# Kernel tuning notes

Hardware: AMD Instinct MI355X
Metric: run time of the kernel (lower is better)

The kernel has to match this reference:

```python
import jax, jax.numpy as jnp
import numpy as np

N, L, C, H, W, HEAD = 16, 256, 512, 32, 32, 16

def setup_inputs() -> dict:
    key = jax.random.key(0)
    ks = jax.random.split(key, 8)
    s = 0.02  # weight init scale
    return {
        "feature": jax.random.normal(ks[0], (N, C, H, W), jnp.float32),
        "token": jax.random.normal(ks[1], (N, L, C), jnp.float32),
        "wq": jax.random.normal(ks[2], (C, C), jnp.float32) * s,
        "bq": jax.random.normal(ks[3], (C,), jnp.float32) * s,
        "wk": jax.random.normal(ks[4], (C, C), jnp.float32) * s,
        "bk": jax.random.normal(ks[5], (C,), jnp.float32) * s,
        "wv": jax.random.normal(ks[6], (C, C), jnp.float32) * s,
        "bv": jax.random.normal(ks[7], (C,), jnp.float32) * s,
    }

def reference(feature, token, wq, bq, wk, bk, wv, bv):
    n, c, hgt, wid = feature.shape
    h = HEAD
    d = c // h
    l = token.shape[1]
    scale = jnp.asarray(np.sqrt(c / h), feature.dtype)
    tok = token.transpose(0, 2, 1)  # (N, C, L)
    # 1x1 conv projections == per-position GEMMs
    v = (jnp.einsum('ncl,dc->ndl', tok, wv) + bv[None, :, None]).reshape(n, h, d, l)
    k = (jnp.einsum('ncl,dc->ndl', tok, wk) + bk[None, :, None]).reshape(n, h, d, l)
    q = (jnp.einsum('nchw,dc->ndhw', feature, wq) + bq[None, :, None, None])
    q = q.reshape(n, h, d, hgt * wid).transpose(0, 1, 3, 2)  # (N, h, HW, d)
    scores = jnp.einsum('nhqd,nhdl->nhql', q, k) / scale  # (N, h, HW, L)
    coef = jax.nn.softmax(scores, axis=-1)
    proj = jnp.einsum('nhdl,nhql->nhdq', v, coef)  # (N, h, d, HW)
    return feature + proj.reshape(n, c, hgt, wid)
```

## Files before the change

### kernel.cpp

```cpp
#include <hip/hip_runtime.h>
#include <hip/hip_bf16.h>

#define N_ 16
#define L_ 256
#define C_ 512
#define HW_ 1024
#define HEADS_ 16
#define DH_ 32

typedef unsigned short u16;
typedef unsigned int u32;
typedef __attribute__((ext_vector_type(8))) short short8_t;
typedef __attribute__((ext_vector_type(4))) float f32x4;

__device__ __forceinline__ u16 f2bs(float f) {
    union { float f; u32 i; } x; x.f = f;
    u32 r = x.i + 0x7fffu + ((x.i >> 16) & 1u);
    return (u16)(r >> 16);
}
__device__ __forceinline__ u32 cvt_pk_bf16(float lo, float hi) {
    u32 r;
    asm("v_cvt_pk_bf16_f32 %0, %1, %2" : "=v"(r) : "v"(lo), "v"(hi));
    return r;
}
#define AS1(p) (const __attribute__((address_space(1))) void*)(p)
#define AS3(p) (__attribute__((address_space(3))) void*)(p)

__global__ __launch_bounds__(256) void prep_kernel(
    const float* __restrict__ token, const float* __restrict__ wq,
    const float* __restrict__ wk, const float* __restrict__ wv,
    const float* __restrict__ feature,
    u16* __restrict__ tokb, u16* __restrict__ wqb,
    u16* __restrict__ wkb, u16* __restrict__ wvb,
    u16* __restrict__ Ftb)
{
    __shared__ float LT[64][67];
    const int t = threadIdx.x;

    if (blockIdx.x < 2816) {
        const int idx = blockIdx.x * 256 + t;
        const float* s; u16* d; int off;
        if (idx < 524288)            { s = token; d = tokb; off = idx; }
        else if (idx < 524288+65536) { s = wq; d = wqb; off = idx - 524288; }
        else if (idx < 524288+131072){ s = wk; d = wkb; off = idx - 524288 - 65536; }
        else                         { s = wv; d = wvb; off = idx - 524288 - 131072; }
        float4 v = ((const float4*)s)[off];
        ushort4 w;
        w.x = f2bs(v.x); w.y = f2bs(v.y); w.z = f2bs(v.z); w.w = f2bs(v.w);
        ((ushort4*)d)[off] = w;
    } else {
        const int tidx = blockIdx.x - 2816;
        const int pb = tidx & 15, cb = (tidx >> 4) & 7, n = tidx >> 7;
        const int c0 = cb * 64, pos0 = pb * 64;

        #pragma unroll
        for (int r = 0; r < 4; ++r) {
            const int c = r * 16 + (t >> 4);
            const int p = (t & 15) * 4;
            float4 v = *(const float4*)&feature[
                ((size_t)n * C_ + c0 + c) * HW_ + pos0 + p];
            LT[c][p] = v.x; LT[c][p+1] = v.y; LT[c][p+2] = v.z; LT[c][p+3] = v.w;
        }
        __syncthreads();
        #pragma unroll
        for (int rep = 0; rep < 2; ++rep) {
            const int pos = (t >> 3) + rep * 32;
            const int c = (t & 7) * 8;
            u16 tmp[8];
            #pragma unroll
            for (int j = 0; j < 8; ++j) tmp[j] = f2bs(LT[c + j][pos]);
            *(short8_t*)&Ftb[(size_t)(n * HW_ + pos0 + pos) * C_ + c0 + c] =
                *(short8_t*)tmp;
        }
    }
}

__global__ __launch_bounds__(256) void gemm_kernel(
    const u16* __restrict__ Ftb, const u16* __restrict__ tokb,
    const u16* __restrict__ wqb, const u16* __restrict__ wkb,
    const u16* __restrict__ wvb,
    const float* __restrict__ bq, const float* __restrict__ bk,
    const float* __restrict__ bv,
    u16* __restrict__ Qout, u16* __restrict__ Kout, u16* __restrict__ Vt)
{
    __shared__ __align__(16) unsigned char smem[65536];

    const int t = threadIdx.x;
    const int lane = t & 63, wid = t >> 6;
    const int i16 = lane & 15, g = lane >> 4;
    const int r8 = t >> 3, gr = t & 7;

    if (blockIdx.x < 256) {
        const int xcd = blockIdx.x & 7, j = blockIdx.x >> 3;
        const int m0 = (xcd * 4 + (j & 3)) * 128;
        const int n0 = (j >> 2) * 64;
        const int wm = wid >> 1, wn = wid & 1;
        u16 (*LTo)[72] = (u16(*)[72])smem;

        f32x4 ak[4][2], av[4][2];
        #pragma unroll
        for (int mt = 0; mt < 4; ++mt)
            #pragma unroll
            for (int nt = 0; nt < 2; ++nt) {
                ak[mt][nt] = (f32x4){0.f, 0.f, 0.f, 0.f};
                av[mt][nt] = (f32x4){0.f, 0.f, 0.f, 0.f};
            }

        #define KV_STAGE(buf, c0) { \
            _Pragma("unroll") \
            for (int p = 0; p < 4; ++p) { \
                const int row = p * 32 + r8; \
                __builtin_amdgcn_global_load_lds( \
                    AS1(tokb + (size_t)(m0 + row) * C_ + (c0) + ((gr ^ (row & 7)) << 3)), \
                    AS3(smem + (buf) * 32768 + (p * 32 + wid * 8) * 128), 16, 0, 0); } \
            _Pragma("unroll") \
            for (int p = 0; p < 2; ++p) { \
                const int row = p * 32 + r8; \
                const int gs = (gr ^ (row & 7)) << 3; \
                __builtin_amdgcn_global_load_lds( \
                    AS1(wkb + (size_t)(n0 + row) * C_ + (c0) + gs), \
                    AS3(smem + (buf) * 32768 + 16384 + (p * 32 + wid * 8) * 128), 16, 0, 0); \
                __builtin_amdgcn_global_load_lds( \
                    AS1(wvb + (size_t)(n0 + row) * C_ + (c0) + gs), \
                    AS3(smem + (buf) * 32768 + 24576 + (p * 32 + wid * 8) * 128), 16, 0, 0); } }

        KV_STAGE(0, 0);
        __syncthreads();
        #pragma unroll
        for (int cs = 0; cs < 8; ++cs) {
            const int cur = cs & 1;
            if (cs < 7) KV_STAGE(cur ^ 1, (cs + 1) * 64);
            const u16* Tok = (const u16*)(smem + cur * 32768);
            const u16* Bk  = (const u16*)(smem + cur * 32768 + 16384);
            const u16* Bv  = (const u16*)(smem + cur * 32768 + 24576);
            #pragma unroll
            for (int ks = 0; ks < 2; ++ks) {
                short8_t a[4], bbk[2], bbv[2];
                #pragma unroll
                for (int mt = 0; mt < 4; ++mt) {
                    const int m = wm * 64 + mt * 16 + i16;
                    a[mt] = *(const short8_t*)&Tok[m * 64 + ((((ks << 2) | g) ^ (m & 7)) << 3)];
                }
                #pragma unroll
                for (int nt = 0; nt < 2; ++nt) {
                    const int d = wn * 32 + nt * 16 + i16;
                    const int sw = d * 64 + ((((ks << 2) | g) ^ (d & 7)) << 3);
                    bbk[nt] = *(const short8_t*)&Bk[sw];
                    bbv[nt] = *(const short8_t*)&Bv[sw];
                }
                #pragma unroll
                for (int mt = 0; mt < 4; ++mt)
                    #pragma unroll
                    for (int nt = 0; nt < 2; ++nt) {
                        ak[mt][nt] = __builtin_amdgcn_mfma_f32_16x16x32_bf16(
                            a[mt], bbk[nt], ak[mt][nt], 0, 0, 0);
                        av[mt][nt] = __builtin_amdgcn_mfma_f32_16x16x32_bf16(
                            a[mt], bbv[nt], av[mt][nt], 0, 0, 0);
                    }
            }
            __syncthreads();
        }
        const int nb = m0 >> 8, l0 = m0 & 255;
        const size_t vtbase = (size_t)nb * C_ * L_;
        #pragma unroll
        for (int nt = 0; nt < 2; ++nt) {
            const int d = n0 + wn * 32 + nt * 16 + i16;
            const float bb = bv[d];
            #pragma unroll
            for (int mt = 0; mt < 4; ++mt) {
                ushort4 w;
                w.x = f2bs(av[mt][nt][0] + bb);
                w.y = f2bs(av[mt][nt][1] + bb);
                w.z = f2bs(av[mt][nt][2] + bb);
                w.w = f2bs(av[mt][nt][3] + bb);
                const int l = l0 + wm * 64 + mt * 16 + g * 4;
                *(ushort4*)&Vt[vtbase + (size_t)d * L_ + l] = w;
            }
        }
        __syncthreads();
        #pragma unroll
        for (int nt = 0; nt < 2; ++nt) {
            const int col = wn * 32 + nt * 16 + i16;
            const float bb = bk[n0 + col];
            #pragma unroll
            for (int mt = 0; mt < 4; ++mt)
                #pragma unroll
                for (int r = 0; r < 4; ++r)
                    LTo[wm * 64 + mt * 16 + g * 4 + r][col] = f2bs(ak[mt][nt][r] + bb);
        }
        __syncthreads();
        #pragma unroll
        for (int rep = 0; rep < 4; ++rep) {
            const int m = (t >> 3) + rep * 32;
            const int cs2 = (t & 7) * 8;
            *(short8_t*)&Kout[(size_t)(m0 + m) * C_ + n0 + cs2] = *(short8_t*)&LTo[m][cs2];
        }
    } else {
        const int qid = blockIdx.x - 256;
        const int xcd = qid & 7, loc = qid >> 3;
        const int m0 = (xcd * 16 + (loc & 15)) * 128;
        const int n0 = (loc >> 4) * 128;
        const int wm = wid >> 1, wn = wid & 1;
        u16 (*LTo)[136] = (u16(*)[136])smem;

        f32x4 aq[4][4];
        #pragma unroll
        for (int mt = 0; mt < 4; ++mt)
            #pragma unroll
            for (int nt = 0; nt < 4; ++nt)
                aq[mt][nt] = (f32x4){0.f, 0.f, 0.f, 0.f};

        #define Q_STAGE(buf, c0) { \
            _Pragma("unroll") \
            for (int p = 0; p < 4; ++p) { \
                const int row = p * 32 + r8; \
                const int gs = (gr ^ (row & 7)) << 3; \
                __builtin_amdgcn_global_load_lds( \
                    AS1(Ftb + (size_t)(m0 + row) * C_ + (c0) + gs), \
                    AS3(smem + (buf) * 32768 + (p * 32 + wid * 8) * 128), 16, 0, 0); \
                __builtin_amdgcn_global_load_lds( \
                    AS1(wqb + (size_t)(n0 + row) * C_ + (c0) + gs), \
                    AS3(smem + (buf) * 32768 + 16384 + (p * 32 + wid * 8) * 128), 16, 0, 0); } }

        Q_STAGE(0, 0);
        __syncthreads();
        #pragma unroll
        for (int cs = 0; cs < 8; ++cs) {
            const int cur = cs & 1;
            if (cs < 7) Q_STAGE(cur ^ 1, (cs + 1) * 64);
            const u16* Ft = (const u16*)(smem + cur * 32768);
            const u16* Bq = (const u16*)(smem + cur * 32768 + 16384);
            #pragma unroll
            for (int ks = 0; ks < 2; ++ks) {
                short8_t a[4], b[4];
                #pragma unroll
                for (int mt = 0; mt < 4; ++mt) {
                    const int m = wm * 64 + mt * 16 + i16;
                    a[mt] = *(const short8_t*)&Ft[m * 64 + ((((ks << 2) | g) ^ (m & 7)) << 3)];
                }
                #pragma unroll
                for (int nt = 0; nt < 4; ++nt) {
                    const int d = wn * 64 + nt * 16 + i16;
                    b[nt] = *(const short8_t*)&Bq[d * 64 + ((((ks << 2) | g) ^ (d & 7)) << 3)];
                }
                #pragma unroll
                for (int mt = 0; mt < 4; ++mt)
                    #pragma unroll
                    for (int nt = 0; nt < 4; ++nt)
                        aq[mt][nt] = __builtin_amdgcn_mfma_f32_16x16x32_bf16(
                            a[mt], b[nt], aq[mt][nt], 0, 0, 0);
            }
            __syncthreads();
        }
        #pragma unroll
        for (int half = 0; half < 2; ++half) {
            __syncthreads();
            if (wm == half) {
                #pragma unroll
                for (int nt = 0; nt < 4; ++nt) {
                    const int col = wn * 64 + nt * 16 + i16;
                    const float bb = bq[n0 + col];
                    #pragma unroll
                    for (int mt = 0; mt < 4; ++mt)
                        #pragma unroll
                        for (int r = 0; r < 4; ++r)
                            LTo[mt * 16 + g * 4 + r][col] = f2bs(aq[mt][nt][r] + bb);
                }
            }
            __syncthreads();
            #pragma unroll
            for (int rep = 0; rep < 4; ++rep) {
                const int row = rep * 16 + (t >> 4);
                const int col = (t & 15) * 8;
                *(short8_t*)&Qout[(size_t)(m0 + half * 64 + row) * C_ + n0 + col] =
                    *(short8_t*)&LTo[row][col];
            }
        }
    }
}

__global__ __launch_bounds__(256) void attn_kernel(
    const u16* __restrict__ Qws, const u16* __restrict__ Kws,
    const u16* __restrict__ Vws, const float* __restrict__ feature,
    float* __restrict__ out)
{
    __shared__ __align__(16) unsigned char smem[32768];

    const int t = threadIdx.x;
    const int wid = t >> 6, lane = t & 63;
    const int i16 = lane & 15, g = lane >> 4;
    const int pt = blockIdx.x, h = blockIdx.y, n = blockIdx.z;
    const int pos0 = pt * 64;
    const size_t qbase = ((size_t)n * HW_ + pos0) * C_ + h * DH_;
    const size_t kbase = ((size_t)n * L_) * C_ + h * DH_;
    const size_t vbase = (size_t)n * C_ * L_ + (size_t)h * DH_ * L_;

    const int q = wid * 16 + i16;

    short8_t bq = *(const short8_t*)&Qws[qbase + (size_t)q * C_ + g * 8];

    #pragma unroll
    for (int p = 0; p < 4; ++p) {
        const int kg = (lane & 3) ^ ((lane >> 3) & 3);
        const int kr = wid * 64 + p * 16 + (lane >> 2);
        const u16* ksrc = Kws + kbase + (size_t)kr * C_ + kg * 8;
        __builtin_amdgcn_global_load_lds(AS1(ksrc),
            AS3(smem + wid * 4096 + p * 1024), 16, 0, 0);
        const int vd = wid * 8 + p * 2 + (lane >> 5);
        const u16* vsrc = Vws + vbase + (size_t)vd * L_ + ((lane & 31) ^ (vd & 7)) * 8;
        __builtin_amdgcn_global_load_lds(AS1(vsrc),
            AS3(smem + 16384 + wid * 4096 + p * 1024), 16, 0, 0);
    }
    __syncthreads();

    const int kgr = g ^ ((i16 >> 1) & 3);
    f32x4 s[16];
    #pragma unroll
    for (int nf = 0; nf < 16; ++nf) {
        short8_t a = *(const short8_t*)(smem + (nf * 16 + i16) * 64 + kgr * 16);
        f32x4 z = {0.f, 0.f, 0.f, 0.f};
        s[nf] = __builtin_amdgcn_mfma_f32_16x16x32_bf16(a, bq, z, 0, 0, 0);
    }

    float mm[16], sm[16];
    #pragma unroll
    for (int nf = 0; nf < 16; ++nf)
        mm[nf] = fmaxf(fmaxf(s[nf][0], s[nf][1]), fmaxf(s[nf][2], s[nf][3]));
    #pragma unroll
    for (int st = 8; st >= 1; st >>= 1)
        #pragma unroll
        for (int i = 0; i < 8; ++i)
            if (i < st) mm[i] = fmaxf(mm[i], mm[i + st]);
    float m = mm[0];
    m = fmaxf(m, __shfl_xor(m, 16));
    m = fmaxf(m, __shfl_xor(m, 32));

    const float K2 = 0.25506288f;
    #pragma unroll
    for (int nf = 0; nf < 16; ++nf) {
        #pragma unroll
        for (int r = 0; r < 4; ++r) s[nf][r] = exp2f((s[nf][r] - m) * K2);
        sm[nf] = (s[nf][0] + s[nf][1]) + (s[nf][2] + s[nf][3]);
    }
    #pragma unroll
    for (int st = 8; st >= 1; st >>= 1)
        #pragma unroll
        for (int i = 0; i < 8; ++i)
            if (i < st) sm[i] += sm[i + st];
    float ssum = sm[0];
    ssum += __shfl_xor(ssum, 16);
    ssum += __shfl_xor(ssum, 32);
    const float pinv = 1.0f / ssum;

    __syncthreads();

    f32x4 o0 = {0.f, 0.f, 0.f, 0.f}, o1 = {0.f, 0.f, 0.f, 0.f};
    const int e7 = i16 & 7;

    #pragma unroll
    for (int hb = 0; hb < 2; ++hb) {
        #pragma unroll
        for (int nfp = 0; nfp < 8; ++nfp) {
            const int nf = hb * 8 + nfp;
            #pragma unroll
            for (int w = 0; w < 2; ++w) {
                u32 pw = cvt_pk_bf16(s[nf][2 * w] * pinv, s[nf][2 * w + 1] * pinv);
                const int gran = (nfp * 2 + (g >> 1)) ^ e7;
                *(u32*)(smem + q * 256 + gran * 16 + ((g & 1) * 2 + w) * 4) = pw;
            }
        }
        __syncthreads();
        #pragma unroll
        for (int ks = 0; ks < 4; ++ks) {
            short8_t pb = *(const short8_t*)(smem + q * 256 + (((ks * 4 + g) ^ e7) * 16));
            const int vg = (((hb * 4 + ks) * 4 + g) ^ e7) * 16;
            short8_t va0 = *(const short8_t*)(smem + 16384 + i16 * 512 + vg);
            short8_t va1 = *(const short8_t*)(smem + 16384 + (16 + i16) * 512 + vg);
            o0 = __builtin_amdgcn_mfma_f32_16x16x32_bf16(va0, pb, o0, 0, 0, 0);
            o1 = __builtin_amdgcn_mfma_f32_16x16x32_bf16(va1, pb, o1, 0, 0, 0);
        }
        if (hb == 0) __syncthreads();
    }

    const size_t obase = ((size_t)n * C_ + h * DH_) * HW_ + pos0 + q;
    #pragma unroll
    for (int r = 0; r < 4; ++r) {
        const size_t oa = obase + (size_t)(g * 4 + r) * HW_;
        out[oa] = feature[oa] + o0[r];
        const size_t ob = obase + (size_t)(16 + g * 4 + r) * HW_;
        out[ob] = feature[ob] + o1[r];
    }
}

extern "C" void kernel_launch(void* const* d_in, const int* in_sizes, int n_in,
                              void* d_out, int out_size, void* d_ws, size_t ws_size,
                              hipStream_t stream)
{
    const float* feature = (const float*)d_in[0];
    const float* token   = (const float*)d_in[1];
    const float* wq      = (const float*)d_in[2];
    const float* bq      = (const float*)d_in[3];
    const float* wk      = (const float*)d_in[4];
    const float* bk      = (const float*)d_in[5];
    const float* wv      = (const float*)d_in[6];
    const float* bv      = (const float*)d_in[7];
    float* out = (float*)d_out;

    u16* Qws = (u16*)d_ws;
    u16* Kws = Qws + (size_t)N_ * HW_ * C_;
    u16* Vws = Kws + (size_t)N_ * L_ * C_;

    char* ob = (char*)d_out;
    u16* Ftb  = (u16*)ob;
    u16* tokb = (u16*)(ob + (16u << 20));
    u16* wkb  = (u16*)(ob + (20u << 20));
    u16* wvb  = (u16*)(ob + (20u << 20) + 524288);
    u16* wqb  = (u16*)(ob + (21u << 20));

    prep_kernel<<<dim3(4864), 256, 0, stream>>>(token, wq, wk, wv, feature,
                                                tokb, wqb, wkb, wvb, Ftb);
    gemm_kernel<<<dim3(768), 256, 0, stream>>>(Ftb, tokb, wqb, wkb, wvb,
                                               bq, bk, bv, Qws, Kws, Vws);
    attn_kernel<<<dim3(16, 16, 16), 256, 0, stream>>>(Qws, Kws, Vws, feature, out);
}
```

Before: 71.43 us.

## Fuse K/V projection with fp32-to-bf16 conversion into prep kernel

The K/V projection GEMM moves into the prep kernel and reads fp32 token and weights directly, converting to bf16 while staging into shared memory. This removes the separate bf16 copies of token, wk and wv and their global round trip. The Q GEMM becomes its own kernel. The fused K/V path drops the async global_load_lds double buffering in favour of synchronous register-staged loads, so it may overlap memory with compute less well. It also now runs concurrently with the feature transpose blocks.

Result: slower. 78.95 us (+10.5%).

```diff
diff --git a/kernel.cpp b/kernel.cpp
--- a/kernel.cpp
+++ b/kernel.cpp
@@ -23,33 +23,33 @@
     asm("v_cvt_pk_bf16_f32 %0, %1, %2" : "=v"(r) : "v"(lo), "v"(hi));
     return r;
 }
+__device__ __forceinline__ void cvt8(const float* __restrict__ src, void* dst) {
+    float4 lo = *(const float4*)src;
+    float4 hi = *(const float4*)(src + 4);
+    union { u32 w[4]; short8_t v; } pk;
+    pk.w[0] = cvt_pk_bf16(lo.x, lo.y);
+    pk.w[1] = cvt_pk_bf16(lo.z, lo.w);
+    pk.w[2] = cvt_pk_bf16(hi.x, hi.y);
+    pk.w[3] = cvt_pk_bf16(hi.z, hi.w);
+    *(short8_t*)dst = pk.v;
+}
 #define AS1(p) (const __attribute__((address_space(1))) void*)(p)
 #define AS3(p) (__attribute__((address_space(3))) void*)(p)
 
-__global__ __launch_bounds__(256) void prep_kernel(
-    const float* __restrict__ token, const float* __restrict__ wq,
-    const float* __restrict__ wk, const float* __restrict__ wv,
-    const float* __restrict__ feature,
-    u16* __restrict__ tokb, u16* __restrict__ wqb,
-    u16* __restrict__ wkb, u16* __restrict__ wvb,
-    u16* __restrict__ Ftb)
+__global__ __launch_bounds__(256) void prep_kv_kernel(
+    const float* __restrict__ feature, const float* __restrict__ token,
+    const float* __restrict__ wq, const float* __restrict__ wk,
+    const float* __restrict__ wv, const float* __restrict__ bk,
+    const float* __restrict__ bv,
+    u16* __restrict__ Ftb, u16* __restrict__ wqb,
+    u16* __restrict__ Kout, u16* __restrict__ Vt)
 {
-    __shared__ float LT[64][67];
+    __shared__ __align__(16) unsigned char smem[32768];
     const int t = threadIdx.x;
 
-    if (blockIdx.x < 2816) {
-        const int idx = blockIdx.x * 256 + t;
-        const float* s; u16* d; int off;
-        if (idx < 524288)            { s = token; d = tokb; off = idx; }
-        else if (idx < 524288+65536) { s = wq; d = wqb; off = idx - 524288; }
-        else if (idx < 524288+131072){ s = wk; d = wkb; off = idx - 524288 - 65536; }
-        else                         { s = wv; d = wvb; off = idx - 524288 - 131072; }
-        float4 v = ((const float4*)s)[off];
-        ushort4 w;
-        w.x = f2bs(v.x); w.y = f2bs(v.y); w.z = f2bs(v.z); w.w = f2bs(v.w);
-        ((ushort4*)d)[off] = w;
-    } else {
-        const int tidx = blockIdx.x - 2816;
+    if (blockIdx.x < 2048) {
+        float (*LT)[67] = (float(*)[67])smem;
+        const int tidx = blockIdx.x;
         const int pb = tidx & 15, cb = (tidx >> 4) & 7, n = tidx >> 7;
         const int c0 = cb * 64, pos0 = pb * 64;
 
@@ -72,29 +72,18 @@
             *(short8_t*)&Ftb[(size_t)(n * HW_ + pos0 + pos) * C_ + c0 + c] =
                 *(short8_t*)tmp;
         }
-    }
-}
-
-__global__ __launch_bounds__(256) void gemm_kernel(
-    const u16* __restrict__ Ftb, const u16* __restrict__ tokb,
-    const u16* __restrict__ wqb, const u16* __restrict__ wkb,
-    const u16* __restrict__ wvb,
-    const float* __restrict__ bq, const float* __restrict__ bk,
-    const float* __restrict__ bv,
-    u16* __restrict__ Qout, u16* __restrict__ Kout, u16* __restrict__ Vt)
-{
-    __shared__ __align__(16) unsigned char smem[65536];
-
-    const int t = threadIdx.x;
-    const int lane = t & 63, wid = t >> 6;
-    const int i16 = lane & 15, g = lane >> 4;
-    const int r8 = t >> 3, gr = t & 7;
-
-    if (blockIdx.x < 256) {
-        const int xcd = blockIdx.x & 7, j = blockIdx.x >> 3;
+    } else if (blockIdx.x < 2304) {
+        const int kvid = blockIdx.x - 2048;
+        const int xcd = kvid & 7, j = kvid >> 3;
         const int m0 = (xcd * 4 + (j & 3)) * 128;
         const int n0 = (j >> 2) * 64;
+        const int lane = t & 63, wid = t >> 6;
+        const int i16 = lane & 15, g = lane >> 4;
         const int wm = wid >> 1, wn = wid & 1;
+        const int r8 = t >> 3, c8 = t & 7;
+        u16* Tok = (u16*)smem;
+        u16* Bk  = (u16*)(smem + 16384);
+        u16* Bv  = (u16*)(smem + 24576);
         u16 (*LTo)[72] = (u16(*)[72])smem;
 
         f32x4 ak[4][2], av[4][2];
@@ -106,33 +95,22 @@
                 av[mt][nt] = (f32x4){0.f, 0.f, 0.f, 0.f};
             }
 
-        #define KV_STAGE(buf, c0) { \
-            _Pragma("unroll") \
-            for (int p = 0; p < 4; ++p) { \
-                const int row = p * 32 + r8; \
-                __builtin_amdgcn_global_load_lds( \
-                    AS1(tokb + (size_t)(m0 + row) * C_ + (c0) + ((gr ^ (row & 7)) << 3)), \
-                    AS3(smem + (buf) * 32768 + (p * 32 + wid * 8) * 128), 16, 0, 0); } \
-            _Pragma("unroll") \
-            for (int p = 0; p < 2; ++p) { \
-                const int row = p * 32 + r8; \
-                const int gs = (gr ^ (row & 7)) << 3; \
-                __builtin_amdgcn_global_load_lds( \
-                    AS1(wkb + (size_t)(n0 + row) * C_ + (c0) + gs), \
-                    AS3(smem + (buf) * 32768 + 16384 + (p * 32 + wid * 8) * 128), 16, 0, 0); \
-                __builtin_amdgcn_global_load_lds( \
-                    AS1(wvb + (size_t)(n0 + row) * C_ + (c0) + gs), \
-                    AS3(smem + (buf) * 32768 + 24576 + (p * 32 + wid * 8) * 128), 16, 0, 0); } }
-
-        KV_STAGE(0, 0);
-        __syncthreads();
-        #pragma unroll
-        for (int cs = 0; cs < 8; ++cs) {
-            const int cur = cs & 1;
-            if (cs < 7) KV_STAGE(cur ^ 1, (cs + 1) * 64);
-            const u16* Tok = (const u16*)(smem + cur * 32768);
-            const u16* Bk  = (const u16*)(smem + cur * 32768 + 16384);
-            const u16* Bv  = (const u16*)(smem + cur * 32768 + 24576);
+        for (int c0 = 0; c0 < C_; c0 += 64) {
+            __syncthreads();
+            #pragma unroll
+            for (int p = 0; p < 4; ++p) {
+                const int m = p * 32 + r8;
+                cvt8(&token[(size_t)(m0 + m) * C_ + c0 + c8 * 8],
+                     &Tok[m * 64 + ((c8 ^ (m & 7)) << 3)]);
+            }
+            #pragma unroll
+            for (int p = 0; p < 2; ++p) {
+                const int m = p * 32 + r8;
+                const int sw = m * 64 + ((c8 ^ (m & 7)) << 3);
+                cvt8(&wk[(size_t)(n0 + m) * C_ + c0 + c8 * 8], &Bk[sw]);
+                cvt8(&wv[(size_t)(n0 + m) * C_ + c0 + c8 * 8], &Bv[sw]);
+            }
+            __syncthreads();
             #pragma unroll
             for (int ks = 0; ks < 2; ++ks) {
                 short8_t a[4], bbk[2], bbv[2];
@@ -158,7 +136,6 @@
                             a[mt], bbv[nt], av[mt][nt], 0, 0, 0);
                     }
             }
-            __syncthreads();
         }
         const int nb = m0 >> 8, l0 = m0 & 255;
         const size_t vtbase = (size_t)nb * C_ * L_;
@@ -196,85 +173,103 @@
             *(short8_t*)&Kout[(size_t)(m0 + m) * C_ + n0 + cs2] = *(short8_t*)&LTo[m][cs2];
         }
     } else {
-        const int qid = blockIdx.x - 256;
-        const int xcd = qid & 7, loc = qid >> 3;
-        const int m0 = (xcd * 16 + (loc & 15)) * 128;
-        const int n0 = (loc >> 4) * 128;
-        const int wm = wid >> 1, wn = wid & 1;
-        u16 (*LTo)[136] = (u16(*)[136])smem;
-
-        f32x4 aq[4][4];
-        #pragma unroll
-        for (int mt = 0; mt < 4; ++mt)
-            #pragma unroll
-            for (int nt = 0; nt < 4; ++nt)
-                aq[mt][nt] = (f32x4){0.f, 0.f, 0.f, 0.f};
-
-        #define Q_STAGE(buf, c0) { \
-            _Pragma("unroll") \
-            for (int p = 0; p < 4; ++p) { \
-                const int row = p * 32 + r8; \
-                const int gs = (gr ^ (row & 7)) << 3; \
-                __builtin_amdgcn_global_load_lds( \
-                    AS1(Ftb + (size_t)(m0 + row) * C_ + (c0) + gs), \
-                    AS3(smem + (buf) * 32768 + (p * 32 + wid * 8) * 128), 16, 0, 0); \
-                __builtin_amdgcn_global_load_lds( \
-                    AS1(wqb + (size_t)(n0 + row) * C_ + (c0) + gs), \
-                    AS3(smem + (buf) * 32768 + 16384 + (p * 32 + wid * 8) * 128), 16, 0, 0); } }
-
-        Q_STAGE(0, 0);
-        __syncthreads();
-        #pragma unroll
-        for (int cs = 0; cs < 8; ++cs) {
-            const int cur = cs & 1;
-            if (cs < 7) Q_STAGE(cur ^ 1, (cs + 1) * 64);
-            const u16* Ft = (const u16*)(smem + cur * 32768);
-            const u16* Bq = (const u16*)(smem + cur * 32768 + 16384);
-            #pragma unroll
-            for (int ks = 0; ks < 2; ++ks) {
-                short8_t a[4], b[4];
-                #pragma unroll
-                for (int mt = 0; mt < 4; ++mt) {
-                    const int m = wm * 64 + mt * 16 + i16;
-                    a[mt] = *(const short8_t*)&Ft[m * 64 + ((((ks << 2) | g) ^ (m & 7)) << 3)];
-                }
-                #pragma unroll
-                for (int nt = 0; nt < 4; ++nt) {
-                    const int d = wn * 64 + nt * 16 + i16;
-                    b[nt] = *(const short8_t*)&Bq[d * 64 + ((((ks << 2) | g) ^ (d & 7)) << 3)];
-                }
+        const int idx = (blockIdx.x - 2304) * 256 + t;
+        float4 v = ((const float4*)wq)[idx];
+        ushort4 w;
+        w.x = f2bs(v.x); w.y = f2bs(v.y); w.z = f2bs(v.z); w.w = f2bs(v.w);
+        ((ushort4*)wqb)[idx] = w;
+    }
+}
+
+__global__ __launch_bounds__(256) void gemm_q_kernel(
+    const u16* __restrict__ Ftb, const u16* __restrict__ wqb,
+    const float* __restrict__ bq, u16* __restrict__ Qout)
+{
+    __shared__ __align__(16) unsigned char smem[65536];
+
+    const int t = threadIdx.x;
+    const int lane = t & 63, wid = t >> 6;
+    const int i16 = lane & 15, g = lane >> 4;
+    const int r8 = t >> 3, gr = t & 7;
+
+    const int qid = blockIdx.x;
+    const int xcd = qid & 7, loc = qid >> 3;
+    const int m0 = (xcd * 16 + (loc & 15)) * 128;
+    const int n0 = (loc >> 4) * 128;
+    const int wm = wid >> 1, wn = wid & 1;
+    u16 (*LTo)[136] = (u16(*)[136])smem;
+
+    f32x4 aq[4][4];
+    #pragma unroll
+    for (int mt = 0; mt < 4; ++mt)
+        #pragma unroll
+        for (int nt = 0; nt < 4; ++nt)
+            aq[mt][nt] = (f32x4){0.f, 0.f, 0.f, 0.f};
+
+    #define Q_STAGE(buf, c0) { \
+        _Pragma("unroll") \
+        for (int p = 0; p < 4; ++p) { \
+            const int row = p * 32 + r8; \
+            const int gs = (gr ^ (row & 7)) << 3; \
+            __builtin_amdgcn_global_load_lds( \
+                AS1(Ftb + (size_t)(m0 + row) * C_ + (c0) + gs), \
+                AS3(smem + (buf) * 32768 + (p * 32 + wid * 8) * 128), 16, 0, 0); \
+            __builtin_amdgcn_global_load_lds( \
+                AS1(wqb + (size_t)(n0 + row) * C_ + (c0) + gs), \
+                AS3(smem + (buf) * 32768 + 16384 + (p * 32 + wid * 8) * 128), 16, 0, 0); } }
+
+    Q_STAGE(0, 0);
+    __syncthreads();
+    #pragma unroll
+    for (int cs = 0; cs < 8; ++cs) {
+        const int cur = cs & 1;
+        if (cs < 7) Q_STAGE(cur ^ 1, (cs + 1) * 64);
+        const u16* Ft = (const u16*)(smem + cur * 32768);
+        const u16* Bq = (const u16*)(smem + cur * 32768 + 16384);
+        #pragma unroll
+        for (int ks = 0; ks < 2; ++ks) {
+            short8_t a[4], b[4];
+            #pragma unroll
+            for (int mt = 0; mt < 4; ++mt) {
+                const int m = wm * 64 + mt * 16 + i16;
+                a[mt] = *(const short8_t*)&Ft[m * 64 + ((((ks << 2) | g) ^ (m & 7)) << 3)];
+            }
+            #pragma unroll
+            for (int nt = 0; nt < 4; ++nt) {
+                const int d = wn * 64 + nt * 16 + i16;
+                b[nt] = *(const short8_t*)&Bq[d * 64 + ((((ks << 2) | g) ^ (d & 7)) << 3)];
+            }
+            #pragma unroll
+            for (int mt = 0; mt < 4; ++mt)
+                #pragma unroll
+                for (int nt = 0; nt < 4; ++nt)
+                    aq[mt][nt] = __builtin_amdgcn_mfma_f32_16x16x32_bf16(
+                        a[mt], b[nt], aq[mt][nt], 0, 0, 0);
+        }
+        __syncthreads();
+    }
+    #pragma unroll
+    for (int half = 0; half < 2; ++half) {
+        __syncthreads();
+        if (wm == half) {
+            #pragma unroll
+            for (int nt = 0; nt < 4; ++nt) {
+                const int col = wn * 64 + nt * 16 + i16;
+                const float bb = bq[n0 + col];
                 #pragma unroll
                 for (int mt = 0; mt < 4; ++mt)
                     #pragma unroll
-                    for (int nt = 0; nt < 4; ++nt)
-                        aq[mt][nt] = __builtin_amdgcn_mfma_f32_16x16x32_bf16(
-                            a[mt], b[nt], aq[mt][nt], 0, 0, 0);
-            }
-            __syncthreads();
-        }
-        #pragma unroll
-        for (int half = 0; half < 2; ++half) {
-            __syncthreads();
-            if (wm == half) {
-                #pragma unroll
-                for (int nt = 0; nt < 4; ++nt) {
-                    const int col = wn * 64 + nt * 16 + i16;
-                    const float bb = bq[n0 + col];
-                    #pragma unroll
-                    for (int mt = 0; mt < 4; ++mt)
-                        #pragma unroll
-                        for (int r = 0; r < 4; ++r)
-                            LTo[mt * 16 + g * 4 + r][col] = f2bs(aq[mt][nt][r] + bb);
-                }
-            }
-            __syncthreads();
-            #pragma unroll
-            for (int rep = 0; rep < 4; ++rep) {
-                const int row = rep * 16 + (t >> 4);
-                const int col = (t & 15) * 8;
-                *(short8_t*)&Qout[(size_t)(m0 + half * 64 + row) * C_ + n0 + col] =
-                    *(short8_t*)&LTo[row][col];
-            }
+                    for (int r = 0; r < 4; ++r)
+                        LTo[mt * 16 + g * 4 + r][col] = f2bs(aq[mt][nt][r] + bb);
+            }
+        }
+        __syncthreads();
+        #pragma unroll
+        for (int rep = 0; rep < 4; ++rep) {
+            const int row = rep * 16 + (t >> 4);
+            const int col = (t & 15) * 8;
+            *(short8_t*)&Qout[(size_t)(m0 + half * 64 + row) * C_ + n0 + col] =
+                *(short8_t*)&LTo[row][col];
         }
     }
 }
@@ -411,15 +406,11 @@
     u16* Vws = Kws + (size_t)N_ * L_ * C_;
 
     char* ob = (char*)d_out;
-    u16* Ftb  = (u16*)ob;
-    u16* tokb = (u16*)(ob + (16u << 20));
-    u16* wkb  = (u16*)(ob + (20u << 20));
-    u16* wvb  = (u16*)(ob + (20u << 20) + 524288);
-    u16* wqb  = (u16*)(ob + (21u << 20));
-
-    prep_kernel<<<dim3(4864), 256, 0, stream>>>(token, wq, wk, wv, feature,
-                                                tokb, wqb, wkb, wvb, Ftb);
-    gemm_kernel<<<dim3(768), 256, 0, stream>>>(Ftb, tokb, wqb, wkb, wvb,
-                                               bq, bk, bv, Qws, Kws, Vws);
+    u16* Ftb = (u16*)ob;
+    u16* wqb = (u16*)(ob + (21u << 20));
+
+    prep_kv_kernel<<<dim3(2560), 256, 0, stream>>>(feature, token, wq, wk, wv,
+                                                   bk, bv, Ftb, wqb, Kws, Vws);
+    gemm_q_kernel<<<dim3(512), 256, 0, stream>>>(Ftb, wqb, bq, Qws);
     attn_kernel<<<dim3(16, 16, 16), 256, 0, stream>>>(Qws, Kws, Vws, feature, out);
 }
```
